# Kernel tuning notes

Measured on AMD Instinct MI355X. Metric: run time of the kernel, lower is better.

The kernel has to match this reference:

```python
import jax, jax.numpy as jnp
import numpy as np

N = 100000      # nodes
E = 1600000     # edges (avg degree 16)
EMB = 64        # embedding_size (per-head out channels)
H = 2           # heads (hardcoded in module)
HID = 128       # hidden_size
NEG_SLOPE = 0.2 # GATv2 default


def setup_inputs() -> dict:
    key = jax.random.key(0)
    ks = jax.random.split(key, 12)
    s = 0.1
    x = jax.random.normal(ks[0], (N, 1), jnp.float32)
    edge_index = jax.random.randint(ks[1], (2, E), 0, N, dtype=jnp.int64)
    edge_attr = jax.random.normal(ks[2], (E, 1), jnp.float32)
    # GATv2Conv params (in_channels=1, out=EMB, heads=H, edge_dim=1)
    W_l = jax.random.normal(ks[3], (1, H * EMB), jnp.float32) * s
    b_l = jnp.zeros((H * EMB,), jnp.float32)
    W_r = jax.random.normal(ks[4], (1, H * EMB), jnp.float32) * s
    b_r = jnp.zeros((H * EMB,), jnp.float32)
    W_e = jax.random.normal(ks[5], (1, H * EMB), jnp.float32) * s   # lin_edge, bias=False
    att = jax.random.normal(ks[6], (H, EMB), jnp.float32) * s       # attention vector a
    bias_out = jnp.zeros((H * EMB,), jnp.float32)                   # conv output bias (concat=True)
    # fc: Linear(embedding_size*4, hidden_size)
    W_fc = jax.random.normal(ks[7], (HID, 4 * EMB), jnp.float32) * s
    b_fc = jnp.zeros((HID,), jnp.float32)
    return {
        "x": x, "edge_index": edge_index, "edge_attr": edge_attr,
        "target_node_idx": 123,
        "W_l": W_l, "b_l": b_l, "W_r": W_r, "b_r": b_r,
        "W_e": W_e, "att": att, "bias_out": bias_out,
        "W_fc": W_fc, "b_fc": b_fc,
    }


def reference(x, edge_index, edge_attr, target_node_idx,
              W_l, b_l, W_r, b_r, W_e, att, bias_out, W_fc, b_fc):
    n = x.shape[0]
    h, c = att.shape
    src, dst = edge_index[0], edge_index[1]

    # add_self_loops with fill_value='mean': per-target-node mean of incoming edge_attr
    deg = jax.ops.segment_sum(jnp.ones((src.shape[0],), x.dtype), dst, num_segments=n)
    attr_mean = jax.ops.segment_sum(edge_attr, dst, num_segments=n) / jnp.maximum(deg, 1.0)[:, None]
    loop = jnp.arange(n, dtype=src.dtype)
    src_f = jnp.concatenate([src, loop])
    dst_f = jnp.concatenate([dst, loop])
    ea = jnp.concatenate([edge_attr, attr_mean], axis=0)  # [E+N, 1]

    # per-head node transforms
    x_l = (x @ W_l + b_l).reshape(n, h, c)  # source transform
    x_r = (x @ W_r + b_r).reshape(n, h, c)  # target transform
    e_edge = (ea @ W_e).reshape(-1, h, c)   # edge-feature transform

    # GATv2: e_ij = a^T LeakyReLU(W_l x_j + W_r x_i + W_e e_ij)
    e = jax.nn.leaky_relu(x_l[src_f] + x_r[dst_f] + e_edge, NEG_SLOPE)  # [E', H, C]
    logits = jnp.einsum('ehc,hc->eh', e, att)  # [E', H]

    # segment softmax over incoming edges per target node
    m = jax.ops.segment_max(logits, dst_f, num_segments=n)     # [N, H]
    expv = jnp.exp(logits - m[dst_f])
    denom = jax.ops.segment_sum(expv, dst_f, num_segments=n)
    alpha = expv / denom[dst_f]                                 # [E', H]

    # weighted scatter-aggregate of source messages, concat heads, add bias
    out = jax.ops.segment_sum(alpha[:, :, None] * x_l[src_f], dst_f, num_segments=n)
    graph_emb = out.reshape(n, h * c) + bias_out                # [N, 2*EMB]

    # gather target, repeat, concat, linear
    tgt = graph_emb[target_node_idx]                            # [2*EMB]
    combined = jnp.concatenate([graph_emb, jnp.broadcast_to(tgt[None, :], graph_emb.shape)], axis=1)
    return combined @ W_fc.T + b_fc                             # [N, HID]
```

## Files before the change

kernel.cpp:

```cpp
#include <hip/hip_runtime.h>
#include <math.h>


#define LRELU_A1 0.6f
#define LRELU_A2 0.4f
#define TB       256
#define EPB      2048
#define NPB      128
#define NB_MAX   1024
#define SB_MAX   1024

__global__ void k_prep(const unsigned int* __restrict__ ei,
                       const float* __restrict__ att,
                       const float* __restrict__ W_l,
                       const float* __restrict__ b_l, const float* __restrict__ b_r,
                       const float* __restrict__ bias_out,
                       const float* __restrict__ W_fc, const float* __restrict__ b_fc,
                       float* __restrict__ C) {
  int j = threadIdx.x;
  unsigned long long nz = __ballot(j < 32 && ei[2 * j + 1] != 0u);
  if (j == 0) ((int*)C)[1024] = (nz == 0ull) ? 1 : 0;
  if (j >= 128) return;
  float a = att[j];
  C[j] = LRELU_A1 * a;
  C[128 + j] = LRELU_A2 * a;
  C[256 + j] = b_l[j] + b_r[j];
  const float* wrow = W_fc + j * 256;
  float u0 = 0.f, u1 = 0.f, v0 = 0.f, v1 = 0.f, cb = b_fc[j];
  for (int c = 0; c < 64; c++) {
    u0 = fmaf(W_l[c],      wrow[c],       u0);
    u1 = fmaf(W_l[64 + c], wrow[64 + c],  u1);
    v0 = fmaf(W_l[c],      wrow[128 + c], v0);
    v1 = fmaf(W_l[64 + c], wrow[192 + c], v1);
  }
  for (int t = 0; t < 128; t++) {
    float gb = b_l[t] + bias_out[t];
    cb = fmaf(gb, wrow[t] + wrow[128 + t], cb);
  }
  C[384 + j] = u0;
  C[512 + j] = u1;
  C[640 + j] = v0;
  C[768 + j] = v1;
  C[896 + j] = cb;
}

#define CH_STEP(comp, ACC, i)                                                      \
  do {                                                                             \
    float v_ = fmaf(xs8[i], wl.comp, fmaf(xt8[i], wr.comp, fmaf(ae8[i], we.comp, bb.comp))); \
    ACC[i] = fmaf(a2.comp, fabsf(v_), fmaf(a1.comp, v_, ACC[i]));                  \
  } while (0)

__global__ __launch_bounds__(TB, 4) void k_bin(
    const float* __restrict__ x, const int* __restrict__ ei,
    const float* __restrict__ ea,
    const float* __restrict__ WL, const float* __restrict__ WR,
    const float* __restrict__ WE, const float* __restrict__ C,
    int4* __restrict__ rec, int* __restrict__ offsT,
    int NB, int S_BLOCKS, int E) {
  __shared__ int cnt[NB_MAX];
  __shared__ int pfx[NB_MAX + 1];
  __shared__ int sc[TB];
  const int tid = threadIdx.x;
  for (int i = tid; i < NB_MAX; i += TB) cnt[i] = 0;
  __syncthreads();

  const int e0 = blockIdx.x * EPB;
  const bool w64 = ((const int*)C)[1024] != 0;
  const float* A1 = C;
  const float* A2 = C + 128;
  const float* BASE = C + 256;

  int de8[8];
  float ae8[8], xs8[8], xt8[8];
  bool ok[8];
#pragma unroll
  for (int i = 0; i < 8; i++) {
    int e = e0 + i * TB + tid;
    ok[i] = (e < E);
    int ee = ok[i] ? e : 0;
    int s_ = w64 ? ei[2 * ee] : ei[ee];
    int d_ = w64 ? ei[2 * (E + ee)] : ei[E + ee];
    de8[i] = d_;
    ae8[i] = ea[ee];
    xs8[i] = x[s_];
    xt8[i] = x[d_];
  }
  float acc0[8] = {0.f, 0.f, 0.f, 0.f, 0.f, 0.f, 0.f, 0.f};
  float acc1[8] = {0.f, 0.f, 0.f, 0.f, 0.f, 0.f, 0.f, 0.f};
#pragma unroll 2
  for (int jb = 0; jb < 64; jb += 4) {
    float4 wl = *(const float4*)(WL + jb);
    float4 wr = *(const float4*)(WR + jb);
    float4 we = *(const float4*)(WE + jb);
    float4 bb = *(const float4*)(BASE + jb);
    float4 a1 = *(const float4*)(A1 + jb);
    float4 a2 = *(const float4*)(A2 + jb);
#pragma unroll
    for (int i = 0; i < 8; i++) {
      CH_STEP(x, acc0, i); CH_STEP(y, acc0, i); CH_STEP(z, acc0, i); CH_STEP(w, acc0, i);
    }
  }
#pragma unroll 2
  for (int jb = 64; jb < 128; jb += 4) {
    float4 wl = *(const float4*)(WL + jb);
    float4 wr = *(const float4*)(WR + jb);
    float4 we = *(const float4*)(WE + jb);
    float4 bb = *(const float4*)(BASE + jb);
    float4 a1 = *(const float4*)(A1 + jb);
    float4 a2 = *(const float4*)(A2 + jb);
#pragma unroll
    for (int i = 0; i < 8; i++) {
      CH_STEP(x, acc1, i); CH_STEP(y, acc1, i); CH_STEP(z, acc1, i); CH_STEP(w, acc1, i);
    }
  }
  int b8[8], slot8[8], p0[8], p1[8], p2[8], p3[8];
#pragma unroll
  for (int i = 0; i < 8; i++) {
    int d_ = de8[i];
    b8[i] = d_ >> 7;
    p0[i] = __float_as_int(__expf(acc0[i]));
    p1[i] = __float_as_int(__expf(acc1[i]));
    p2[i] = __float_as_int(xs8[i]);
    p3[i] = (int)((__float_as_uint(ae8[i]) & ~127u) | (unsigned)(d_ & 127));
    slot8[i] = ok[i] ? atomicAdd(&cnt[b8[i]], 1) : 0;
  }
  __syncthreads();
  int l4[4], mysum = 0;
#pragma unroll
  for (int j = 0; j < 4; j++) {
    int idx = tid * 4 + j;
    l4[j] = (idx < NB) ? cnt[idx] : 0;
    mysum += l4[j];
  }
  sc[tid] = mysum;
  __syncthreads();
  for (int st = 1; st < TB; st <<= 1) {
    int v = (tid >= st) ? sc[tid - st] : 0;
    __syncthreads();
    sc[tid] += v;
    __syncthreads();
  }
  int run = sc[tid] - mysum;
#pragma unroll
  for (int j = 0; j < 4; j++) {
    int idx = tid * 4 + j;
    if (idx < NB) { pfx[idx] = run; run += l4[j]; }
  }
  if (tid == 0) pfx[NB] = sc[TB - 1];
  __syncthreads();
  for (int b = tid; b <= NB; b += TB)
    offsT[(size_t)b * S_BLOCKS + blockIdx.x] = pfx[b];
  int4* myrec = rec + (size_t)blockIdx.x * EPB;
#pragma unroll
  for (int i = 0; i < 8; i++) {
    if (ok[i]) myrec[pfx[b8[i]] + slot8[i]] = make_int4(p0[i], p1[i], p2[i], p3[i]);
  }
}

__global__ __launch_bounds__(TB, 4) void k_reduce(
    const float* __restrict__ x,
    const float* __restrict__ WL, const float* __restrict__ WR,
    const float* __restrict__ WE, const float* __restrict__ C,
    const int4* __restrict__ rec, const int* __restrict__ offsT,
    float* __restrict__ S, int S_BLOCKS, int N) {
  __shared__ float lacc[NPB * 7];
  __shared__ int sstart[SB_MAX];
  __shared__ int spfx[SB_MAX];
  __shared__ int sc[TB];
  const int tid = threadIdx.x;
  const int b = blockIdx.x;
  for (int i = tid; i < NPB * 7; i += TB) lacc[i] = 0.f;
  int l4[4], st4[4], mysum = 0;
#pragma unroll
  for (int j = 0; j < 4; j++) {
    int s = tid * 4 + j;
    int st = 0, len = 0;
    if (s < S_BLOCKS) {
      st  = offsT[(size_t)b * S_BLOCKS + s];
      len = offsT[(size_t)(b + 1) * S_BLOCKS + s] - st;
    }
    st4[j] = st; l4[j] = len; mysum += len;
  }
  sc[tid] = mysum;
  __syncthreads();
  for (int st = 1; st < TB; st <<= 1) {
    int v = (tid >= st) ? sc[tid - st] : 0;
    __syncthreads();
    sc[tid] += v;
    __syncthreads();
  }
  int run = sc[tid] - mysum;
#pragma unroll
  for (int j = 0; j < 4; j++) {
    int s = tid * 4 + j;
    if (s < S_BLOCKS) { sstart[s] = st4[j]; run += l4[j]; spfx[s] = run; }
  }
  __syncthreads();
  const int T = sc[TB - 1];
  for (int i = tid; i < T; i += TB) {
    int lo = 0, hi = S_BLOCKS - 1;
    while (lo < hi) { int mid = (lo + hi) >> 1; if (spfx[mid] > i) hi = mid; else lo = mid + 1; }
    int base = (lo == 0) ? 0 : spfx[lo - 1];
    int4 r = rec[(size_t)lo * EPB + sstart[lo] + (i - base)];
    float e0v = __int_as_float(r.x);
    float e1v = __int_as_float(r.y);
    float xsv = __int_as_float(r.z);
    unsigned eab = (unsigned)r.w;
    float* a = lacc + (int)(eab & 127u) * 7;
    float aev = __uint_as_float(eab & ~127u);
    atomicAdd(a + 0, e0v);
    atomicAdd(a + 1, e0v * xsv);
    atomicAdd(a + 2, e1v);
    atomicAdd(a + 3, e1v * xsv);
    atomicAdd(a + 4, aev);
    atomicAdd(a + 5, 1.0f);
  }
  __syncthreads();
  const int n = b * NPB + tid;
  if (tid < NPB && n < N) {
    const float* la = lacc + tid * 7;
    float den0 = la[0], num0 = la[1], den1 = la[2], num1 = la[3];
    float asum = la[4], cntv = la[5];
    const float* A1 = C;
    const float* A2 = C + 128;
    const float* BASE = C + 256;
    float xn = x[n];
    float am = asum / fmaxf(cntv, 1.0f);
    float acc0 = 0.f, acc1 = 0.f;
#pragma unroll 4
    for (int jb = 0; jb < 64; jb += 4) {
      float4 wl = *(const float4*)(WL + jb);
      float4 wr = *(const float4*)(WR + jb);
      float4 we = *(const float4*)(WE + jb);
      float4 bb = *(const float4*)(BASE + jb);
      float4 a1 = *(const float4*)(A1 + jb);
      float4 a2 = *(const float4*)(A2 + jb);
      float v;
      v = fmaf(xn, wl.x + wr.x, fmaf(am, we.x, bb.x)); acc0 = fmaf(a2.x, fabsf(v), fmaf(a1.x, v, acc0));
      v = fmaf(xn, wl.y + wr.y, fmaf(am, we.y, bb.y)); acc0 = fmaf(a2.y, fabsf(v), fmaf(a1.y, v, acc0));
      v = fmaf(xn, wl.z + wr.z, fmaf(am, we.z, bb.z)); acc0 = fmaf(a2.z, fabsf(v), fmaf(a1.z, v, acc0));
      v = fmaf(xn, wl.w + wr.w, fmaf(am, we.w, bb.w)); acc0 = fmaf(a2.w, fabsf(v), fmaf(a1.w, v, acc0));
    }
#pragma unroll 4
    for (int jb = 64; jb < 128; jb += 4) {
      float4 wl = *(const float4*)(WL + jb);
      float4 wr = *(const float4*)(WR + jb);
      float4 we = *(const float4*)(WE + jb);
      float4 bb = *(const float4*)(BASE + jb);
      float4 a1 = *(const float4*)(A1 + jb);
      float4 a2 = *(const float4*)(A2 + jb);
      float v;
      v = fmaf(xn, wl.x + wr.x, fmaf(am, we.x, bb.x)); acc1 = fmaf(a2.x, fabsf(v), fmaf(a1.x, v, acc1));
      v = fmaf(xn, wl.y + wr.y, fmaf(am, we.y, bb.y)); acc1 = fmaf(a2.y, fabsf(v), fmaf(a1.y, v, acc1));
      v = fmaf(xn, wl.z + wr.z, fmaf(am, we.z, bb.z)); acc1 = fmaf(a2.z, fabsf(v), fmaf(a1.z, v, acc1));
      v = fmaf(xn, wl.w + wr.w, fmaf(am, we.w, bb.w)); acc1 = fmaf(a2.w, fabsf(v), fmaf(a1.w, v, acc1));
    }
    float s0 = __expf(acc0), s1 = __expf(acc1);
    float2 sv;
    sv.x = (num0 + s0 * xn) / (den0 + s0);
    sv.y = (num1 + s1 * xn) / (den1 + s1);
    *(float2*)(S + 2 * n) = sv;
  }
}

__global__ __launch_bounds__(256) void k_out(
    const float* __restrict__ S, const float* __restrict__ C,
    const int* __restrict__ tgtp, float* __restrict__ out, int N) {
  int g = blockIdx.x * blockDim.x + threadIdx.x;
  if (g >= N * 32) return;
  int n = g >> 5;
  int kq = (g & 31) * 4;
  int T = tgtp[0];
  float s0t = S[2 * T], s1t = S[2 * T + 1];
  float2 s = *(const float2*)(S + 2 * n);
  float4 u0 = *(const float4*)(C + 384 + kq);
  float4 u1 = *(const float4*)(C + 512 + kq);
  float4 v0 = *(const float4*)(C + 640 + kq);
  float4 v1 = *(const float4*)(C + 768 + kq);
  float4 cb = *(const float4*)(C + 896 + kq);
  float4 o;
  o.x = fmaf(s.x, u0.x, fmaf(s.y, u1.x, fmaf(s0t, v0.x, fmaf(s1t, v1.x, cb.x))));
  o.y = fmaf(s.x, u0.y, fmaf(s.y, u1.y, fmaf(s0t, v0.y, fmaf(s1t, v1.y, cb.y))));
  o.z = fmaf(s.x, u0.z, fmaf(s.y, u1.z, fmaf(s0t, v0.z, fmaf(s1t, v1.z, cb.z))));
  o.w = fmaf(s.x, u0.w, fmaf(s.y, u1.w, fmaf(s0t, v0.w, fmaf(s1t, v1.w, cb.w))));
  *(float4*)(out + n * 128 + kq) = o;
}

extern "C" void kernel_launch(void* const* d_in, const int* in_sizes, int n_in,
                              void* d_out, int out_size, void* d_ws, size_t ws_size,
                              hipStream_t stream) {
  const float* x        = (const float*)d_in[0];
  const int*   ei       = (const int*)d_in[1];
  const float* ea       = (const float*)d_in[2];
  const int*   tgt      = (const int*)d_in[3];
  const float* W_l      = (const float*)d_in[4];
  const float* b_l      = (const float*)d_in[5];
  const float* W_r      = (const float*)d_in[6];
  const float* b_r      = (const float*)d_in[7];
  const float* W_e      = (const float*)d_in[8];
  const float* att      = (const float*)d_in[9];
  const float* bias_out = (const float*)d_in[10];
  const float* W_fc     = (const float*)d_in[11];
  const float* b_fc     = (const float*)d_in[12];

  const int N = in_sizes[0];
  const int E = in_sizes[2];
  const int NB = (N + NPB - 1) / NPB;
  const int S_BLOCKS = (E + EPB - 1) / EPB;

  char* p = (char*)d_ws;
  int4*  rec   = (int4*)p;                      p += (size_t)S_BLOCKS * EPB * 16;
  int*   offsT = (int*)p;                       p += (size_t)(NB + 1) * S_BLOCKS * 4;
  float* S     = (float*)p;                     p += (size_t)2 * N * 4;
  float* C     = (float*)p;

  k_prep<<<1, 128, 0, stream>>>((const unsigned int*)ei, att, W_l, b_l, b_r,
                                bias_out, W_fc, b_fc, C);
  k_bin<<<S_BLOCKS, TB, 0, stream>>>(x, ei, ea, W_l, W_r, W_e, C,
                                     rec, offsT, NB, S_BLOCKS, E);
  k_reduce<<<NB, TB, 0, stream>>>(x, W_l, W_r, W_e, C, rec, offsT, S,
                                  S_BLOCKS, N);
  k_out<<<(N * 32 + 255) / 256, 256, 0, stream>>>(S, C, tgt, (float*)d_out, N);
}
```

Before: 242.5 us.

## Split per-node reduction across source-bin partitions and replace binary search with LUT

The reduce kernel now runs on a 2D grid where each block handles only a slice (P parts) of the source bins for its node bucket, writing partial sums to a workspace buffer. A new finalize kernel sums the partials and computes the self-loop attention and normalized output. Per-edge binary search over bin prefixes is replaced by a shared-memory index LUT filled in windows. This gives more parallelism for the roughly 782 node blocks and cheaper address computation, at the cost of an extra kernel launch, partial-sum traffic and additional workspace.

```diff
diff --git a/kernel.cpp b/kernel.cpp
--- a/kernel.cpp
+++ b/kernel.cpp
@@ -9,6 +9,7 @@
 #define NPB      128
 #define NB_MAX   1024
 #define SB_MAX   1024
+#define LUTSZ    2048
 
 __global__ void k_prep(const unsigned int* __restrict__ ei,
                        const float* __restrict__ att,
@@ -157,110 +158,136 @@
   }
 }
 
-__global__ __launch_bounds__(TB, 4) void k_reduce(
+__global__ __launch_bounds__(TB, 8) void k_reduce(
+    const int4* __restrict__ rec, const int* __restrict__ offsT,
+    float* __restrict__ Spart, int S_BLOCKS, int SPP) {
+  __shared__ float lacc[NPB * 7];
+  __shared__ int sc[TB];
+  __shared__ int lut[LUTSZ];
+  const int tid = threadIdx.x;
+  const int b = blockIdx.x;
+  const int part = blockIdx.y;
+  for (int i = tid; i < NPB * 7; i += TB) lacc[i] = 0.f;
+
+  int l4[4], rb4[4];
+  int mysum = 0;
+#pragma unroll
+  for (int j = 0; j < 4; j++) {
+    int sidx = tid * 4 + j;
+    int s = part * SPP + sidx;
+    int st = 0, len = 0;
+    if (sidx < SPP && s < S_BLOCKS) {
+      st  = offsT[(size_t)b * S_BLOCKS + s];
+      len = offsT[(size_t)(b + 1) * S_BLOCKS + s] - st;
+    }
+    rb4[j] = s * EPB + st;
+    l4[j] = len;
+    mysum += len;
+  }
+  sc[tid] = mysum;
+  __syncthreads();
+  for (int d = 1; d < TB; d <<= 1) {
+    int v = (tid >= d) ? sc[tid - d] : 0;
+    __syncthreads();
+    sc[tid] += v;
+    __syncthreads();
+  }
+  const int T = sc[TB - 1];
+  int run = sc[tid] - mysum;
+  int bs4[4];
+#pragma unroll
+  for (int j = 0; j < 4; j++) { bs4[j] = run; run += l4[j]; }
+
+  for (int w0 = 0; w0 < T; w0 += LUTSZ) {
+    const int w1 = min(w0 + LUTSZ, T);
+#pragma unroll
+    for (int j = 0; j < 4; j++) {
+      int lo = max(bs4[j], w0), hi = min(bs4[j] + l4[j], w1);
+      for (int k = lo; k < hi; k++) lut[k - w0] = rb4[j] + (k - bs4[j]);
+    }
+    __syncthreads();
+    for (int i = w0 + tid; i < w1; i += TB) {
+      int4 r = rec[(size_t)(unsigned)lut[i - w0]];
+      float e0v = __int_as_float(r.x);
+      float e1v = __int_as_float(r.y);
+      float xsv = __int_as_float(r.z);
+      unsigned eab = (unsigned)r.w;
+      float* a = lacc + (int)(eab & 127u) * 7;
+      float aev = __uint_as_float(eab & ~127u);
+      atomicAdd(a + 0, e0v);
+      atomicAdd(a + 1, e0v * xsv);
+      atomicAdd(a + 2, e1v);
+      atomicAdd(a + 3, e1v * xsv);
+      atomicAdd(a + 4, aev);
+      atomicAdd(a + 5, 1.0f);
+    }
+    __syncthreads();
+  }
+  __syncthreads();
+  float* out = Spart + ((size_t)b * gridDim.y + part) * (NPB * 6);
+  for (int u = tid; u < NPB * 6; u += TB)
+    out[u] = lacc[(u / 6) * 7 + (u % 6)];
+}
+
+__global__ __launch_bounds__(256) void k_fin(
     const float* __restrict__ x,
     const float* __restrict__ WL, const float* __restrict__ WR,
     const float* __restrict__ WE, const float* __restrict__ C,
-    const int4* __restrict__ rec, const int* __restrict__ offsT,
-    float* __restrict__ S, int S_BLOCKS, int N) {
-  __shared__ float lacc[NPB * 7];
-  __shared__ int sstart[SB_MAX];
-  __shared__ int spfx[SB_MAX];
-  __shared__ int sc[TB];
-  const int tid = threadIdx.x;
-  const int b = blockIdx.x;
-  for (int i = tid; i < NPB * 7; i += TB) lacc[i] = 0.f;
-  int l4[4], st4[4], mysum = 0;
-#pragma unroll
-  for (int j = 0; j < 4; j++) {
-    int s = tid * 4 + j;
-    int st = 0, len = 0;
-    if (s < S_BLOCKS) {
-      st  = offsT[(size_t)b * S_BLOCKS + s];
-      len = offsT[(size_t)(b + 1) * S_BLOCKS + s] - st;
-    }
-    st4[j] = st; l4[j] = len; mysum += len;
-  }
-  sc[tid] = mysum;
-  __syncthreads();
-  for (int st = 1; st < TB; st <<= 1) {
-    int v = (tid >= st) ? sc[tid - st] : 0;
-    __syncthreads();
-    sc[tid] += v;
-    __syncthreads();
-  }
-  int run = sc[tid] - mysum;
-#pragma unroll
-  for (int j = 0; j < 4; j++) {
-    int s = tid * 4 + j;
-    if (s < S_BLOCKS) { sstart[s] = st4[j]; run += l4[j]; spfx[s] = run; }
-  }
-  __syncthreads();
-  const int T = sc[TB - 1];
-  for (int i = tid; i < T; i += TB) {
-    int lo = 0, hi = S_BLOCKS - 1;
-    while (lo < hi) { int mid = (lo + hi) >> 1; if (spfx[mid] > i) hi = mid; else lo = mid + 1; }
-    int base = (lo == 0) ? 0 : spfx[lo - 1];
-    int4 r = rec[(size_t)lo * EPB + sstart[lo] + (i - base)];
-    float e0v = __int_as_float(r.x);
-    float e1v = __int_as_float(r.y);
-    float xsv = __int_as_float(r.z);
-    unsigned eab = (unsigned)r.w;
-    float* a = lacc + (int)(eab & 127u) * 7;
-    float aev = __uint_as_float(eab & ~127u);
-    atomicAdd(a + 0, e0v);
-    atomicAdd(a + 1, e0v * xsv);
-    atomicAdd(a + 2, e1v);
-    atomicAdd(a + 3, e1v * xsv);
-    atomicAdd(a + 4, aev);
-    atomicAdd(a + 5, 1.0f);
-  }
-  __syncthreads();
-  const int n = b * NPB + tid;
-  if (tid < NPB && n < N) {
-    const float* la = lacc + tid * 7;
-    float den0 = la[0], num0 = la[1], den1 = la[2], num1 = la[3];
-    float asum = la[4], cntv = la[5];
-    const float* A1 = C;
-    const float* A2 = C + 128;
-    const float* BASE = C + 256;
-    float xn = x[n];
-    float am = asum / fmaxf(cntv, 1.0f);
-    float acc0 = 0.f, acc1 = 0.f;
+    const float* __restrict__ Spart, float* __restrict__ S,
+    int N, int P) {
+  int n = blockIdx.x * blockDim.x + threadIdx.x;
+  if (n >= N) return;
+  int b = n >> 7, t = n & 127;
+  const float* q0 = Spart + ((size_t)b * P) * (NPB * 6) + t * 6;
+  float den0 = 0.f, num0 = 0.f, den1 = 0.f, num1 = 0.f, asum = 0.f, cntv = 0.f;
+  for (int p = 0; p < P; p++) {
+    const float* q = q0 + (size_t)p * (NPB * 6);
+    float2 v0 = *(const float2*)(q);
+    float2 v1 = *(const float2*)(q + 2);
+    float2 v2 = *(const float2*)(q + 4);
+    den0 += v0.x; num0 += v0.y;
+    den1 += v1.x; num1 += v1.y;
+    asum += v2.x; cntv += v2.y;
+  }
+  const float* A1 = C;
+  const float* A2 = C + 128;
+  const float* BASE = C + 256;
+  float xn = x[n];
+  float am = asum / fmaxf(cntv, 1.0f);
+  float acc0 = 0.f, acc1 = 0.f;
 #pragma unroll 4
-    for (int jb = 0; jb < 64; jb += 4) {
-      float4 wl = *(const float4*)(WL + jb);
-      float4 wr = *(const float4*)(WR + jb);
-      float4 we = *(const float4*)(WE + jb);
-      float4 bb = *(const float4*)(BASE + jb);
-      float4 a1 = *(const float4*)(A1 + jb);
-      float4 a2 = *(const float4*)(A2 + jb);
-      float v;
-      v = fmaf(xn, wl.x + wr.x, fmaf(am, we.x, bb.x)); acc0 = fmaf(a2.x, fabsf(v), fmaf(a1.x, v, acc0));
-      v = fmaf(xn, wl.y + wr.y, fmaf(am, we.y, bb.y)); acc0 = fmaf(a2.y, fabsf(v), fmaf(a1.y, v, acc0));
-      v = fmaf(xn, wl.z + wr.z, fmaf(am, we.z, bb.z)); acc0 = fmaf(a2.z, fabsf(v), fmaf(a1.z, v, acc0));
-      v = fmaf(xn, wl.w + wr.w, fmaf(am, we.w, bb.w)); acc0 = fmaf(a2.w, fabsf(v), fmaf(a1.w, v, acc0));
-    }
+  for (int jb = 0; jb < 64; jb += 4) {
+    float4 wl = *(const float4*)(WL + jb);
+    float4 wr = *(const float4*)(WR + jb);
+    float4 we = *(const float4*)(WE + jb);
+    float4 bb = *(const float4*)(BASE + jb);
+    float4 a1 = *(const float4*)(A1 + jb);
+    float4 a2 = *(const float4*)(A2 + jb);
+    float v;
+    v = fmaf(xn, wl.x + wr.x, fmaf(am, we.x, bb.x)); acc0 = fmaf(a2.x, fabsf(v), fmaf(a1.x, v, acc0));
+    v = fmaf(xn, wl.y + wr.y, fmaf(am, we.y, bb.y)); acc0 = fmaf(a2.y, fabsf(v), fmaf(a1.y, v, acc0));
+    v = fmaf(xn, wl.z + wr.z, fmaf(am, we.z, bb.z)); acc0 = fmaf(a2.z, fabsf(v), fmaf(a1.z, v, acc0));
+    v = fmaf(xn, wl.w + wr.w, fmaf(am, we.w, bb.w)); acc0 = fmaf(a2.w, fabsf(v), fmaf(a1.w, v, acc0));
+  }
 #pragma unroll 4
-    for (int jb = 64; jb < 128; jb += 4) {
-      float4 wl = *(const float4*)(WL + jb);
-      float4 wr = *(const float4*)(WR + jb);
-      float4 we = *(const float4*)(WE + jb);
-      float4 bb = *(const float4*)(BASE + jb);
-      float4 a1 = *(const float4*)(A1 + jb);
-      float4 a2 = *(const float4*)(A2 + jb);
-      float v;
-      v = fmaf(xn, wl.x + wr.x, fmaf(am, we.x, bb.x)); acc1 = fmaf(a2.x, fabsf(v), fmaf(a1.x, v, acc1));
-      v = fmaf(xn, wl.y + wr.y, fmaf(am, we.y, bb.y)); acc1 = fmaf(a2.y, fabsf(v), fmaf(a1.y, v, acc1));
-      v = fmaf(xn, wl.z + wr.z, fmaf(am, we.z, bb.z)); acc1 = fmaf(a2.z, fabsf(v), fmaf(a1.z, v, acc1));
-      v = fmaf(xn, wl.w + wr.w, fmaf(am, we.w, bb.w)); acc1 = fmaf(a2.w, fabsf(v), fmaf(a1.w, v, acc1));
-    }
-    float s0 = __expf(acc0), s1 = __expf(acc1);
-    float2 sv;
-    sv.x = (num0 + s0 * xn) / (den0 + s0);
-    sv.y = (num1 + s1 * xn) / (den1 + s1);
-    *(float2*)(S + 2 * n) = sv;
-  }
+  for (int jb = 64; jb < 128; jb += 4) {
+    float4 wl = *(const float4*)(WL + jb);
+    float4 wr = *(const float4*)(WR + jb);
+    float4 we = *(const float4*)(WE + jb);
+    float4 bb = *(const float4*)(BASE + jb);
+    float4 a1 = *(const float4*)(A1 + jb);
+    float4 a2 = *(const float4*)(A2 + jb);
+    float v;
+    v = fmaf(xn, wl.x + wr.x, fmaf(am, we.x, bb.x)); acc1 = fmaf(a2.x, fabsf(v), fmaf(a1.x, v, acc1));
+    v = fmaf(xn, wl.y + wr.y, fmaf(am, we.y, bb.y)); acc1 = fmaf(a2.y, fabsf(v), fmaf(a1.y, v, acc1));
+    v = fmaf(xn, wl.z + wr.z, fmaf(am, we.z, bb.z)); acc1 = fmaf(a2.z, fabsf(v), fmaf(a1.z, v, acc1));
+    v = fmaf(xn, wl.w + wr.w, fmaf(am, we.w, bb.w)); acc1 = fmaf(a2.w, fabsf(v), fmaf(a1.w, v, acc1));
+  }
+  float s0 = __expf(acc0), s1 = __expf(acc1);
+  float2 sv;
+  sv.x = (num0 + s0 * xn) / (den0 + s0);
+  sv.y = (num1 + s1 * xn) / (den1 + s1);
+  *(float2*)(S + 2 * n) = sv;
 }
 
 __global__ __launch_bounds__(256) void k_out(
@@ -308,17 +335,28 @@
   const int NB = (N + NPB - 1) / NPB;
   const int S_BLOCKS = (E + EPB - 1) / EPB;
 
+  const size_t sz_rec  = (size_t)S_BLOCKS * EPB * 16;
+  const size_t sz_offs = (size_t)(NB + 1) * S_BLOCKS * 4;
+  const size_t sz_S    = (size_t)2 * N * 4;
+  const size_t sz_C    = 4608;
+  int P = 4;
+  while (P > 1 &&
+         sz_rec + sz_offs + sz_S + sz_C + (size_t)NB * P * NPB * 6 * 4 > ws_size)
+    P >>= 1;
+  const int SPP = (S_BLOCKS + P - 1) / P;
+
   char* p = (char*)d_ws;
-  int4*  rec   = (int4*)p;                      p += (size_t)S_BLOCKS * EPB * 16;
-  int*   offsT = (int*)p;                       p += (size_t)(NB + 1) * S_BLOCKS * 4;
-  float* S     = (float*)p;                     p += (size_t)2 * N * 4;
-  float* C     = (float*)p;
+  int4*  rec   = (int4*)p;                      p += sz_rec;
+  int*   offsT = (int*)p;                       p += sz_offs;
+  float* S     = (float*)p;                     p += sz_S;
+  float* C     = (float*)p;                     p += sz_C;
+  float* Spart = (float*)p;
 
   k_prep<<<1, 128, 0, stream>>>((const unsigned int*)ei, att, W_l, b_l, b_r,
                                 bias_out, W_fc, b_fc, C);
   k_bin<<<S_BLOCKS, TB, 0, stream>>>(x, ei, ea, W_l, W_r, W_e, C,
                                      rec, offsT, NB, S_BLOCKS, E);
-  k_reduce<<<NB, TB, 0, stream>>>(x, W_l, W_r, W_e, C, rec, offsT, S,
-                                  S_BLOCKS, N);
+  k_reduce<<<dim3(NB, P), TB, 0, stream>>>(rec, offsT, Spart, S_BLOCKS, SPP);
+  k_fin<<<(N + 255) / 256, 256, 0, stream>>>(x, W_l, W_r, W_e, C, Spart, S, N, P);
   k_out<<<(N * 32 + 255) / 256, 256, 0, stream>>>(S, C, tgt, (float*)d_out, N);
 }
```

New measurement: 254.5 us. 5.0% more time.
